# Optimization experiments

Hardware: AMD Instinct MI355X
Metric: run time of the kernel (lower is better)

## Reference

```python
import jax, jax.numpy as jnp
import numpy as np

N_NODES = 50000
N_EDGES = 800000
HEADS = 5
NFEAT = 5
C1 = 32  # hidden_layers


def setup_inputs() -> dict:
    key = jax.random.key(0)
    ks = jax.random.split(key, 20)
    s = 0.3  # glorot-ish scale
    d = {
        "x": jax.random.normal(ks[0], (N_NODES, NFEAT), jnp.float32),
        "edge_attr": jax.random.uniform(ks[1], (N_EDGES, 1), jnp.float32),
        "src": jax.random.randint(ks[2], (N_EDGES,), 0, N_NODES, jnp.int32),
        "dst": jax.random.randint(ks[3], (N_EDGES,), 0, N_NODES, jnp.int32),
        # conv1: in=5 -> heads=5, out=32, concat
        "W1": jax.random.normal(ks[4], (NFEAT, HEADS * C1), jnp.float32) * s,
        "a_src1": jax.random.normal(ks[5], (HEADS, C1), jnp.float32) * s,
        "a_dst1": jax.random.normal(ks[6], (HEADS, C1), jnp.float32) * s,
        "We1": jax.random.normal(ks[7], (1, HEADS * C1), jnp.float32) * s,
        "ae1": jax.random.normal(ks[8], (HEADS, C1), jnp.float32) * s,
        "b1": jnp.zeros((HEADS * C1,), jnp.float32),
        # conv2: in=160 -> heads=5, out=1, mean over heads
        "W2": jax.random.normal(ks[9], (HEADS * C1, HEADS * 1), jnp.float32) * 0.08,
        "a_src2": jax.random.normal(ks[10], (HEADS, 1), jnp.float32) * s,
        "a_dst2": jax.random.normal(ks[11], (HEADS, 1), jnp.float32) * s,
        "We2": jax.random.normal(ks[12], (1, HEADS * 1), jnp.float32) * s,
        "ae2": jax.random.normal(ks[13], (HEADS, 1), jnp.float32) * s,
        "b2": jnp.zeros((1,), jnp.float32),
        "Wlin": jax.random.normal(ks[14], (1, 1), jnp.float32),
    }
    return d


def gat_layer(x, src, dst, eattr, W, a_src, a_dst, We, a_e, bias, concat, n_nodes):
    """PyG GATConv with edge_dim, self-loops already added by caller."""
    H, C = a_src.shape
    h = (x @ W).reshape(-1, H, C)                      # [N,H,C]
    alpha_s = (h * a_src[None]).sum(-1)                # [N,H]
    alpha_d = (h * a_dst[None]).sum(-1)                # [N,H]
    ee = (eattr @ We).reshape(-1, H, C)                # [E,H,C]
    alpha_e = (ee * a_e[None]).sum(-1)                 # [E,H]
    logits = jax.nn.leaky_relu(alpha_s[src] + alpha_d[dst] + alpha_e, 0.2)
    # segment softmax over destination nodes
    m = jax.ops.segment_max(logits, dst, num_segments=n_nodes)
    m = jnp.where(jnp.isfinite(m), m, 0.0)
    ex = jnp.exp(logits - m[dst])
    denom = jax.ops.segment_sum(ex, dst, num_segments=n_nodes)
    alpha = ex / (denom[dst] + 1e-16)                  # [E,H]
    msg = (alpha[:, :, None] * h[src]).reshape(-1, H * C)
    agg = jax.ops.segment_sum(msg, dst, num_segments=n_nodes).reshape(n_nodes, H, C)
    if concat:
        return agg.reshape(n_nodes, H * C) + bias
    return agg.mean(axis=1) + bias


def reference(x, edge_attr, src, dst, W1, a_src1, a_dst1, We1, ae1, b1,
              W2, a_src2, a_dst2, We2, ae2, b2, Wlin):
    n = x.shape[0]
    loop = jnp.arange(n, dtype=src.dtype)
    s = jnp.concatenate([src, loop])
    t = jnp.concatenate([dst, loop])
    # self-loop edge_attr = mean of edge_attr (PyG fill_value='mean')
    ea_loop = jnp.broadcast_to(edge_attr.mean(axis=0, keepdims=True), (n, edge_attr.shape[1]))
    ea = jnp.concatenate([edge_attr, ea_loop], axis=0)

    x1 = gat_layer(x, s, t, ea, W1, a_src1, a_dst1, We1, ae1, b1, True, n)
    x2 = jax.nn.relu(x1)
    # dropout p=0.2 is identity in eval mode
    x4 = gat_layer(x2, s, t, ea, W2, a_src2, a_dst2, We2, ae2, b2, False, n)
    x5 = x4 @ Wlin                                     # Linear(1,1,bias=False)
    return jax.nn.sigmoid(x5)                          # [N,1]
```

## Files before the change

kernel.cpp:

```cpp
#include <hip/hip_runtime.h>
#include <hip/hip_fp16.h>
#include <math.h>

#define N_NODES 50000
#define N_EDGES 800000
#define E2 (N_EDGES + N_NODES)
#define HEADS 5
#define C1 32
#define F1 160

#define BSZ 64
#define NBK 782
#define NBL 128
#define CH  6641
#define MTOT (NBK*NBL)
#define MC  391
#define GRID_H1 (N_NODES/4)
#define CAP 1408

#define AGG1_NPB 32
#define AGG1_NB  1563

static constexpr size_t alignup(size_t x){ return (x + 255) & ~size_t(255); }
static constexpr size_t OFF_SCAL  = 0;
static constexpr size_t OFF_H     = alignup(OFF_SCAL + 64*4);
static constexpr size_t OFF_EAS   = alignup(OFF_H    + (size_t)MTOT*4);
static constexpr size_t OFF_PART  = alignup(OFF_EAS  + (size_t)NBL*4);
static constexpr size_t OFF_PPREF = alignup(OFF_PART + (size_t)MC*4);
static constexpr size_t OFF_BST   = alignup(OFF_PPREF+ (size_t)MC*4);
static constexpr size_t OFF_OFFS  = alignup(OFF_BST  + (size_t)(NBK+1)*4);
static constexpr size_t OFF_BPACK = alignup(OFF_OFFS + (size_t)(N_NODES+1)*4);
static constexpr size_t OFF_EDG   = alignup(OFF_BPACK+ (size_t)E2*8);
static constexpr size_t OFF_AS1P  = alignup(OFF_EDG  + (size_t)E2*4);
static constexpr size_t OFF_AD1P  = alignup(OFF_AS1P + (size_t)N_NODES*8*4);
static constexpr size_t OFF_G16   = alignup(OFF_AD1P + (size_t)N_NODES*8*4);
static constexpr size_t OFF_AD2P  = alignup(OFF_G16  + (size_t)N_NODES*16*2);
static constexpr size_t OFF_H1Q   = alignup(OFF_AD2P + (size_t)N_NODES*8*4);
static constexpr size_t OFF_X2H   = alignup(OFF_H1Q  + (size_t)N_NODES*F1);

typedef float vf2 __attribute__((ext_vector_type(2)));
__device__ __forceinline__ float4 fp8x4_to_f32(unsigned int r){
  vf2 lo = __builtin_amdgcn_cvt_pk_f32_fp8((int)r, false);
  vf2 hi = __builtin_amdgcn_cvt_pk_f32_fp8((int)r, true);
  return make_float4(lo.x, lo.y, hi.x, hi.y);
}

__global__ __launch_bounds__(320) void k_init(const float* __restrict__ x, const float* __restrict__ W1,
                       const float* __restrict__ as1w, const float* __restrict__ ad1w,
                       unsigned short* __restrict__ h1qh, float* __restrict__ as1ph, float* __restrict__ ad1ph,
                       const int* __restrict__ dst, const float* __restrict__ ea,
                       int* __restrict__ H, float* __restrict__ easum){
  __shared__ float sW[5*F1];
  int t = threadIdx.x;
  if (blockIdx.x < GRID_H1){
    for (int k = t; k < 5*F1; k += 320) sW[k] = W1[k];
    __syncthreads();
    int nl = t / 80;
    int c  = t - nl*80;
    int n  = blockIdx.x*4 + nl;
    int c0 = 2*c;
    float hv0 = 0.f, hv1 = 0.f;
    #pragma unroll
    for (int f = 0; f < 5; f++){
      float xv = x[n*5 + f];
      hv0 += xv * sW[f*F1 + c0];
      hv1 += xv * sW[f*F1 + c0 + 1];
    }
    int pk = __builtin_amdgcn_cvt_pk_fp8_f32(hv0, hv1, 0, false);
    int hh = c >> 4, pp = c & 15;
    h1qh[(size_t)hh*(N_NODES*16) + n*16 + pp] = (unsigned short)(pk & 0xFFFF);
    float vs = hv0*as1w[c0] + hv1*as1w[c0+1];
    float vd = hv0*ad1w[c0] + hv1*ad1w[c0+1];
    #pragma unroll
    for (int m = 8; m >= 1; m >>= 1){
      vs += __shfl_xor(vs, m, 64);
      vd += __shfl_xor(vd, m, 64);
    }
    if ((c & 15) == 0){
      int h = c >> 4;
      as1ph[h*N_NODES + n] = vs;
      ad1ph[h*N_NODES + n] = vd;
    }
  } else {
    int* hist = (int*)sW;
    float* wsum = (float*)&hist[NBK + 1];
    for (int k = t; k < NBK; k += 320) hist[k] = 0;
    __syncthreads();
    int b = blockIdx.x - GRID_H1;
    int e0 = b*CH, e1 = min(e0 + CH, E2);
    float s = 0.f;
    for (int e = e0 + t; e < e1; e += 320){
      int d;
      if (e < N_EDGES){ d = dst[e]; s += ea[e]; }
      else d = e - N_EDGES;
      atomicAdd(&hist[d >> 6], 1);
    }
    #pragma unroll
    for (int m = 1; m < 64; m <<= 1) s += __shfl_xor(s, m, 64);
    if ((t & 63) == 0) wsum[t >> 6] = s;
    __syncthreads();
    for (int k = t; k < NBK; k += 320) H[(size_t)k*NBL + b] = hist[k];
    if (t == 0) easum[b] = wsum[0] + wsum[1] + wsum[2] + wsum[3] + wsum[4];
  }
}

__global__ void k_s1(const int* __restrict__ H, int* __restrict__ partial){
  int i = blockIdx.x*256 + threadIdx.x;
  int v = (i < MTOT) ? H[i] : 0;
  #pragma unroll
  for (int m = 1; m < 64; m <<= 1) v += __shfl_xor(v, m, 64);
  __shared__ int sh[4];
  if ((threadIdx.x & 63) == 0) sh[threadIdx.x >> 6] = v;
  __syncthreads();
  if (threadIdx.x == 0) partial[blockIdx.x] = sh[0] + sh[1] + sh[2] + sh[3];
}

__global__ __launch_bounds__(512) void k_s2p(const int* __restrict__ partial, int* __restrict__ ppref,
                      int* __restrict__ offs, int* __restrict__ bstart,
                      const float* __restrict__ easum,
                      const float* __restrict__ We1, const float* __restrict__ ae1,
                      const float* __restrict__ We2, const float* __restrict__ ae2,
                      float* __restrict__ scal){
  __shared__ int sp[512];
  __shared__ float sh_ea[NBL];
  int t = threadIdx.x;
  if (t < NBL) sh_ea[t] = easum[t];
  if (t >= 448 && t < 448 + HEADS){
    int h = t - 448;
    float s = 0.f;
    for (int c = 0; c < C1; c++) s += We1[h*C1 + c] * ae1[h*C1 + c];
    scal[2 + h] = s;
    scal[7 + h] = We2[h] * ae2[h];
  }
  int v = (t < MC) ? partial[t] : 0;
  sp[t] = v;
  __syncthreads();
  if (t == 511){
    float es = 0.f;
    for (int i = 0; i < NBL; i++) es += sh_ea[i];
    scal[1] = es / (float)N_EDGES;
  }
  for (int off = 1; off < 512; off <<= 1){
    int u = (t >= off) ? sp[t - off] : 0;
    __syncthreads();
    sp[t] += u;
    __syncthreads();
  }
  if (t < MC) ppref[t] = sp[t] - v;
  if (t == 0){ offs[N_NODES] = E2; bstart[NBK] = E2; }
}

__global__ void k_s3(int* __restrict__ H, const int* __restrict__ ppref, int* __restrict__ bstart){
  __shared__ int sp[256];
  int b = blockIdx.x, t = threadIdx.x;
  int i = b*256 + t;
  int v = (i < MTOT) ? H[i] : 0;
  sp[t] = v;
  __syncthreads();
  for (int off = 1; off < 256; off <<= 1){
    int u = (t >= off) ? sp[t - off] : 0;
    __syncthreads();
    sp[t] += u;
    __syncthreads();
  }
  int P = ppref[b] + sp[t] - v;
  if (i < MTOT){
    H[i] = P;
    if (i % NBL == 0) bstart[i / NBL] = P;
  }
}

__global__ __launch_bounds__(256) void k_scat(const int* __restrict__ src, const int* __restrict__ dst,
                       const float* __restrict__ ea, const float* __restrict__ scal,
                       const int* __restrict__ H, int2* __restrict__ bpack){
  __shared__ int lofs[NBK];
  int b = blockIdx.x;
  for (int k = threadIdx.x; k < NBK; k += 256) lofs[k] = H[(size_t)k*NBL + b];
  __syncthreads();
  float mean = scal[1];
  int e0 = b*CH, e1 = min(e0 + CH, E2);
  for (int e = e0 + threadIdx.x; e < e1; e += 256){
    int d, s; float a;
    if (e < N_EDGES){ d = dst[e]; s = src[e]; a = ea[e]; }
    else { d = s = e - N_EDGES; a = mean; }
    int pos = atomicAdd(&lofs[d >> 6], 1);
    bpack[pos] = make_int2(s | ((d & 63) << 16), __float_as_int(a));
  }
}

__global__ __launch_bounds__(256) void k_final2(const int* __restrict__ bstart,
                        const int2* __restrict__ bpack,
                        int* __restrict__ offs, unsigned int* __restrict__ edge2){
  __shared__ int cnt[BSZ], cur[BSZ];
  __shared__ unsigned int s_edge[CAP];
  int k = blockIdx.x, t = threadIdx.x;
  int base = k*BSZ;
  if (t < BSZ) cnt[t] = 0;
  __syncthreads();
  int r0 = bstart[k], r1 = bstart[k + 1];
  int sz = r1 - r0;
  for (int j = r0 + t; j < r1; j += 256) atomicAdd(&cnt[(bpack[j].x >> 16) & 63], 1);
  __syncthreads();
  if (t == 0){
    int run = 0;
    for (int i = 0; i < BSZ; i++){ int c = cnt[i]; cnt[i] = run; cur[i] = run; run += c; }
  }
  __syncthreads();
  if (t < BSZ){
    int n = base + t;
    if (n < N_NODES) offs[n] = r0 + cnt[t];
  }
  if (sz <= CAP){
    for (int j = r0 + t; j < r1; j += 256){
      int2 v = bpack[j];
      int lp = atomicAdd(&cur[(v.x >> 16) & 63], 1);
      s_edge[lp] = (unsigned int)(v.x & 0xFFFF) |
                   ((unsigned int)__half_as_ushort(__float2half(__int_as_float(v.y))) << 16);
    }
    __syncthreads();
    for (int i = t; i < sz; i += 256) edge2[r0 + i] = s_edge[i];
  } else {
    for (int j = r0 + t; j < r1; j += 256){
      int2 v = bpack[j];
      int pos = r0 + atomicAdd(&cur[(v.x >> 16) & 63], 1);
      edge2[pos] = (unsigned int)(v.x & 0xFFFF) |
                   ((unsigned int)__half_as_ushort(__float2half(__int_as_float(v.y))) << 16);
    }
  }
}

__global__ __launch_bounds__(256) void k_agg1(const int* __restrict__ offs,
                      const unsigned int* __restrict__ edge2,
                      const float* __restrict__ as1ph, const float* __restrict__ ad1ph,
                      const float* __restrict__ scal,
                      const unsigned short* __restrict__ h1qh,
                      const float* __restrict__ b1, __half* __restrict__ x2h){
  int head = blockIdx.x / AGG1_NB;
  int nb   = blockIdx.x - head*AGG1_NB;
  int gl   = threadIdx.x >> 3;
  int q    = threadIdx.x & 7;
  int n    = nb*AGG1_NPB + gl;
  if (n >= N_NODES) return;
  float wd  = scal[2 + head];
  float adn = ad1ph[head*N_NODES + n];
  const float* asn = as1ph + head*N_NODES;
  const unsigned int* h1row = (const unsigned int*)h1qh + (size_t)head*(N_NODES*8) + q;
  int j0 = offs[n], j1 = offs[n + 1];
  float a0 = 0.f, a1 = 0.f, a2 = 0.f, a3 = 0.f, den = 0.f;
  int j = j0;
  for (; j + 7 < j1; j += 8){
    uint4 sa = *(const uint4*)(edge2 + j);
    uint4 sb = *(const uint4*)(edge2 + j + 4);
    unsigned int e0 = sa.x, e1 = sa.y, e2v = sa.z, e3 = sa.w;
    unsigned int e4 = sb.x, e5 = sb.y, e6 = sb.z, e7 = sb.w;
    int s0 = e0 & 0xFFFF, s1 = e1 & 0xFFFF, s2 = e2v & 0xFFFF, s3 = e3 & 0xFFFF;
    int s4 = e4 & 0xFFFF, s5 = e5 & 0xFFFF, s6 = e6 & 0xFFFF, s7 = e7 & 0xFFFF;
    unsigned int r0 = h1row[s0*8];
    unsigned int r1 = h1row[s1*8];
    unsigned int r2 = h1row[s2*8];
    unsigned int r3 = h1row[s3*8];
    unsigned int r4 = h1row[s4*8];
    unsigned int r5 = h1row[s5*8];
    unsigned int r6 = h1row[s6*8];
    unsigned int r7 = h1row[s7*8];
    float g0 = asn[s0], g1 = asn[s1];
    float g2 = asn[s2], g3 = asn[s3];
    float g4 = asn[s4], g5 = asn[s5];
    float g6 = asn[s6], g7 = asn[s7];
    float c0 = __half2float(__ushort_as_half((unsigned short)(e0 >> 16)));
    float c1 = __half2float(__ushort_as_half((unsigned short)(e1 >> 16)));
    float c2 = __half2float(__ushort_as_half((unsigned short)(e2v >> 16)));
    float c3 = __half2float(__ushort_as_half((unsigned short)(e3 >> 16)));
    float c4v = __half2float(__ushort_as_half((unsigned short)(e4 >> 16)));
    float c5v = __half2float(__ushort_as_half((unsigned short)(e5 >> 16)));
    float c6 = __half2float(__ushort_as_half((unsigned short)(e6 >> 16)));
    float c7 = __half2float(__ushort_as_half((unsigned short)(e7 >> 16)));
    float l0 = g0 + adn + c0*wd;  l0 = fminf(fmaxf(l0, 0.2f*l0), 10.f);
    float l1 = g1 + adn + c1*wd;  l1 = fminf(fmaxf(l1, 0.2f*l1), 10.f);
    float l2 = g2 + adn + c2*wd;  l2 = fminf(fmaxf(l2, 0.2f*l2), 10.f);
    float l3 = g3 + adn + c3*wd;  l3 = fminf(fmaxf(l3, 0.2f*l3), 10.f);
    float l4 = g4 + adn + c4v*wd; l4 = fminf(fmaxf(l4, 0.2f*l4), 10.f);
    float l5 = g5 + adn + c5v*wd; l5 = fminf(fmaxf(l5, 0.2f*l5), 10.f);
    float l6 = g6 + adn + c6*wd;  l6 = fminf(fmaxf(l6, 0.2f*l6), 10.f);
    float l7 = g7 + adn + c7*wd;  l7 = fminf(fmaxf(l7, 0.2f*l7), 10.f);
    float p0 = __expf(l0), p1 = __expf(l1), p2 = __expf(l2), p3 = __expf(l3);
    float p4 = __expf(l4), p5 = __expf(l5), p6 = __expf(l6), p7 = __expf(l7);
    den += p0 + p1 + p2 + p3 + p4 + p5 + p6 + p7;
    float4 f0 = fp8x4_to_f32(r0), f1 = fp8x4_to_f32(r1);
    float4 f2 = fp8x4_to_f32(r2), f3 = fp8x4_to_f32(r3);
    float4 f4 = fp8x4_to_f32(r4), f5 = fp8x4_to_f32(r5);
    float4 f6 = fp8x4_to_f32(r6), f7 = fp8x4_to_f32(r7);
    a0 += p0*f0.x; a1 += p0*f0.y; a2 += p0*f0.z; a3 += p0*f0.w;
    a0 += p1*f1.x; a1 += p1*f1.y; a2 += p1*f1.z; a3 += p1*f1.w;
    a0 += p2*f2.x; a1 += p2*f2.y; a2 += p2*f2.z; a3 += p2*f2.w;
    a0 += p3*f3.x; a1 += p3*f3.y; a2 += p3*f3.z; a3 += p3*f3.w;
    a0 += p4*f4.x; a1 += p4*f4.y; a2 += p4*f4.z; a3 += p4*f4.w;
    a0 += p5*f5.x; a1 += p5*f5.y; a2 += p5*f5.z; a3 += p5*f5.w;
    a0 += p6*f6.x; a1 += p6*f6.y; a2 += p6*f6.z; a3 += p6*f6.w;
    a0 += p7*f7.x; a1 += p7*f7.y; a2 += p7*f7.z; a3 += p7*f7.w;
  }
  for (; j < j1; ++j){
    unsigned int e = edge2[j];
    int s = e & 0xFFFF;
    float c = __half2float(__ushort_as_half((unsigned short)(e >> 16)));
    float g = asn[s];
    float lg = g + adn + c*wd;
    lg = fminf(fmaxf(lg, 0.2f*lg), 10.f);
    float p = __expf(lg);
    den += p;
    float4 f = fp8x4_to_f32(h1row[s*8]);
    a0 += p*f.x; a1 += p*f.y; a2 += p*f.z; a3 += p*f.w;
  }
  float inv = 1.f / (den + 1e-16f);
  float4 bb = *(const float4*)(b1 + head*C1 + 4*q);
  float v0 = fmaxf(a0*inv + bb.x, 0.f);
  float v1 = fmaxf(a1*inv + bb.y, 0.f);
  float v2 = fmaxf(a2*inv + bb.z, 0.f);
  float v3 = fmaxf(a3*inv + bb.w, 0.f);
  __half2 o0 = __floats2half2_rn(v0, v1);
  __half2 o1 = __floats2half2_rn(v2, v3);
  *(uint2*)(x2h + (size_t)n*F1 + head*C1 + 4*q) =
      make_uint2(*(unsigned int*)&o0, *(unsigned int*)&o1);
}

__global__ __launch_bounds__(256) void k_h2(const __half* __restrict__ x2h, const float* __restrict__ W2,
                    const float* __restrict__ asw2, const float* __restrict__ adw2,
                    __half* __restrict__ G16, float* __restrict__ ad2p){
  __shared__ float sW[F1*HEADS];
  for (int k = threadIdx.x; k < F1*HEADS; k += 256) sW[k] = W2[k];
  __syncthreads();
  int w = threadIdx.x >> 6, l = threadIdx.x & 63;
  int n = blockIdx.x*4 + w;
  const __half2* x22 = (const __half2*)x2h;
  float acc[HEADS] = {0.f, 0.f, 0.f, 0.f, 0.f};
  for (int k2 = l; k2 < 80; k2 += 64){
    float2 f = __half22float2(x22[(size_t)n*80 + k2]);
    #pragma unroll
    for (int h = 0; h < HEADS; h++)
      acc[h] += f.x * sW[(2*k2)*HEADS + h] + f.y * sW[(2*k2+1)*HEADS + h];
  }
  #pragma unroll
  for (int m = 1; m < 64; m <<= 1){
    #pragma unroll
    for (int h = 0; h < HEADS; h++) acc[h] += __shfl_xor(acc[h], m, 64);
  }
  if (l == 0){
    #pragma unroll
    for (int h = 0; h < HEADS; h++){
      G16[(size_t)n*16 + h]     = __float2half(acc[h]);
      G16[(size_t)n*16 + 5 + h] = __float2half(acc[h] * asw2[h]);
      ad2p[n*8 + h]             = acc[h] * adw2[h];
    }
    #pragma unroll
    for (int z = 10; z < 16; z++) G16[(size_t)n*16 + z] = __float2half(0.f);
  }
}

__global__ __launch_bounds__(256) void k_agg2(const int* __restrict__ offs,
                      const unsigned int* __restrict__ edge2,
                      const __half* __restrict__ G16, const float* __restrict__ ad2p,
                      const float* __restrict__ scal,
                      const float* __restrict__ b2, const float* __restrict__ Wlin,
                      float* __restrict__ out){
  int grp = threadIdx.x >> 4;
  int l16 = threadIdx.x & 15;
  int n = blockIdx.x*16 + grp;
  float adn[HEADS], wd[HEADS];
  #pragma unroll
  for (int h = 0; h < HEADS; h++){ adn[h] = ad2p[n*8 + h]; wd[h] = scal[7 + h]; }
  int j0 = offs[n], j1 = offs[n + 1];

  float den[HEADS] = {0,0,0,0,0};
  float ac[HEADS]  = {0,0,0,0,0};
  for (int j = j0 + l16; j < j1; j += 16){
    unsigned int e = edge2[j];
    int s = e & 0xFFFF;
    float c = __half2float(__ushort_as_half((unsigned short)(e >> 16)));
    const __half* gs = G16 + (size_t)s*16;
    union { uint4 u; __half2 h[4]; } U; U.u = *(const uint4*)gs;
    union { uint2 u; __half2 h[2]; } V; V.u = *(const uint2*)(gs + 8);
    float2 p01 = __half22float2(U.h[0]);
    float2 p23 = __half22float2(U.h[1]);
    float2 p45 = __half22float2(U.h[2]);
    float2 p67 = __half22float2(U.h[3]);
    float2 p89 = __half22float2(V.h[0]);
    float hv[HEADS] = {p01.x, p01.y, p23.x, p23.y, p45.x};
    float av[HEADS] = {p45.y, p67.x, p67.y, p89.x, p89.y};
    #pragma unroll
    for (int h = 0; h < HEADS; h++){
      float lg = av[h] + adn[h] + c*wd[h];
      lg = fmaxf(lg, 0.2f*lg);
      lg = fminf(lg, 50.f);
      float p = __expf(lg);
      den[h] += p;
      ac[h]  += p * hv[h];
    }
  }
  #pragma unroll
  for (int m = 1; m < 16; m <<= 1){
    #pragma unroll
    for (int h = 0; h < HEADS; h++){
      den[h] += __shfl_xor(den[h], m, 16);
      ac[h]  += __shfl_xor(ac[h], m, 16);
    }
  }
  if (l16 == 0){
    float v = 0.f;
    #pragma unroll
    for (int h = 0; h < HEADS; h++) v += ac[h] / (den[h] + 1e-16f);
    v = v * (1.f/HEADS) + b2[0];
    v *= Wlin[0];
    out[n] = 1.f / (1.f + __expf(-v));
  }
}

extern "C" void kernel_launch(void* const* d_in, const int* in_sizes, int n_in,
                              void* d_out, int out_size, void* d_ws, size_t ws_size,
                              hipStream_t stream) {
  const float* x    = (const float*)d_in[0];
  const float* ea   = (const float*)d_in[1];
  const int*   src  = (const int*)d_in[2];
  const int*   dst  = (const int*)d_in[3];
  const float* W1   = (const float*)d_in[4];
  const float* as1w = (const float*)d_in[5];
  const float* ad1w = (const float*)d_in[6];
  const float* We1  = (const float*)d_in[7];
  const float* ae1  = (const float*)d_in[8];
  const float* b1   = (const float*)d_in[9];
  const float* W2   = (const float*)d_in[10];
  const float* as2w = (const float*)d_in[11];
  const float* ad2w = (const float*)d_in[12];
  const float* We2  = (const float*)d_in[13];
  const float* ae2  = (const float*)d_in[14];
  const float* b2   = (const float*)d_in[15];
  const float* Wlin = (const float*)d_in[16];

  char* ws = (char*)d_ws;
  float* scal   = (float*)(ws + OFF_SCAL);
  int*   H      = (int*)  (ws + OFF_H);
  float* easum  = (float*)(ws + OFF_EAS);
  int*   part   = (int*)  (ws + OFF_PART);
  int*   ppref  = (int*)  (ws + OFF_PPREF);
  int*   bstart = (int*)  (ws + OFF_BST);
  int*   offs   = (int*)  (ws + OFF_OFFS);
  int2*  bpack  = (int2*) (ws + OFF_BPACK);
  unsigned int* edge2 = (unsigned int*)(ws + OFF_EDG);
  float* as1ph  = (float*)(ws + OFF_AS1P);
  float* ad1ph  = (float*)(ws + OFF_AD1P);
  __half* G16   = (__half*)(ws + OFF_G16);
  float* ad2p   = (float*)(ws + OFF_AD2P);
  unsigned short* h1qh = (unsigned short*)(ws + OFF_H1Q);
  __half* x2h   = (__half*)(ws + OFF_X2H);
  float* outp   = (float*)d_out;

  k_init   <<<GRID_H1 + NBL, 320, 0, stream>>>(x, W1, as1w, ad1w, h1qh, as1ph, ad1ph,
                                               dst, ea, H, easum);
  k_s1     <<<MC, 256, 0, stream>>>(H, part);
  k_s2p    <<<1, 512, 0, stream>>>(part, ppref, offs, bstart, easum, We1, ae1, We2, ae2, scal);
  k_s3     <<<MC, 256, 0, stream>>>(H, ppref, bstart);
  k_scat   <<<NBL, 256, 0, stream>>>(src, dst, ea, scal, H, bpack);
  k_final2 <<<NBK, 256, 0, stream>>>(bstart, bpack, offs, edge2);

  k_agg1   <<<HEADS*AGG1_NB, 256, 0, stream>>>(offs, edge2, as1ph, ad1ph, scal, h1qh, b1, x2h);
  k_h2     <<<N_NODES/4, 256, 0, stream>>>(x2h, W2, as2w, ad2w, G16, ad2p);
  k_agg2   <<<N_NODES/16, 256, 0, stream>>>(offs, edge2, G16, ad2p, scal, b2, Wlin, outp);
}
```

Baseline: 225.9 us.

## Precompute per-edge attention weights for all heads in a separate logit kernel

Adds a k_logit kernel that computes exp(leaky_relu logits) for all five heads once per edge. It stores them as fp16 packed with the source index in per-head edge arrays, reusing the bpack region and a new P2 buffer. k_agg1 then reads the precomputed weights instead of gathering alpha_src and recomputing exp per head. Per-node alpha values are stored as packed fp16 rows of 8, so one 16-byte load fetches all heads. The trade is an extra kernel launch, about 17MB of extra writes and reads, and fp16 rounding of the attention weights and alpha values.

```diff
diff --git a/kernel.cpp b/kernel.cpp
--- a/kernel.cpp
+++ b/kernel.cpp
@@ -31,12 +31,13 @@
 static constexpr size_t OFF_OFFS  = alignup(OFF_BST  + (size_t)(NBK+1)*4);
 static constexpr size_t OFF_BPACK = alignup(OFF_OFFS + (size_t)(N_NODES+1)*4);
 static constexpr size_t OFF_EDG   = alignup(OFF_BPACK+ (size_t)E2*8);
-static constexpr size_t OFF_AS1P  = alignup(OFF_EDG  + (size_t)E2*4);
-static constexpr size_t OFF_AD1P  = alignup(OFF_AS1P + (size_t)N_NODES*8*4);
-static constexpr size_t OFF_G16   = alignup(OFF_AD1P + (size_t)N_NODES*8*4);
+static constexpr size_t OFF_AS16  = alignup(OFF_EDG  + (size_t)E2*4);
+static constexpr size_t OFF_AD16  = alignup(OFF_AS16 + (size_t)N_NODES*8*2);
+static constexpr size_t OFF_G16   = alignup(OFF_AD16 + (size_t)N_NODES*8*2);
 static constexpr size_t OFF_AD2P  = alignup(OFF_G16  + (size_t)N_NODES*16*2);
 static constexpr size_t OFF_H1Q   = alignup(OFF_AD2P + (size_t)N_NODES*8*4);
 static constexpr size_t OFF_X2H   = alignup(OFF_H1Q  + (size_t)N_NODES*F1);
+static constexpr size_t OFF_P2    = alignup(OFF_X2H  + (size_t)N_NODES*F1*2);
 
 typedef float vf2 __attribute__((ext_vector_type(2)));
 __device__ __forceinline__ float4 fp8x4_to_f32(unsigned int r){
@@ -47,7 +48,7 @@
 
 __global__ __launch_bounds__(320) void k_init(const float* __restrict__ x, const float* __restrict__ W1,
                        const float* __restrict__ as1w, const float* __restrict__ ad1w,
-                       unsigned short* __restrict__ h1qh, float* __restrict__ as1ph, float* __restrict__ ad1ph,
+                       unsigned short* __restrict__ h1qh, __half* __restrict__ as16, __half* __restrict__ ad16,
                        const int* __restrict__ dst, const float* __restrict__ ea,
                        int* __restrict__ H, float* __restrict__ easum){
   __shared__ float sW[5*F1];
@@ -78,8 +79,8 @@
     }
     if ((c & 15) == 0){
       int h = c >> 4;
-      as1ph[h*N_NODES + n] = vs;
-      ad1ph[h*N_NODES + n] = vd;
+      as16[n*8 + h] = __float2half(vs);
+      ad16[n*8 + h] = __float2half(vd);
     }
   } else {
     int* hist = (int*)sW;
@@ -229,10 +230,47 @@
   }
 }
 
+__global__ __launch_bounds__(256) void k_logit(const int* __restrict__ offs,
+                      const unsigned int* __restrict__ edge2,
+                      const __half* __restrict__ as16, const __half* __restrict__ ad16,
+                      const float* __restrict__ scal,
+                      unsigned int* __restrict__ P01, unsigned int* __restrict__ P2){
+  int gl = threadIdx.x >> 3;
+  int q  = threadIdx.x & 7;
+  int n  = blockIdx.x*AGG1_NPB + gl;
+  if (n >= N_NODES) return;
+  union { uint4 u; __half2 h[4]; } AD; AD.u = *(const uint4*)(ad16 + (size_t)n*8);
+  float ad0 = __low2float(AD.h[0]), ad1 = __high2float(AD.h[0]);
+  float ad2 = __low2float(AD.h[1]), ad3 = __high2float(AD.h[1]);
+  float ad4 = __low2float(AD.h[2]);
+  float wd0 = scal[2], wd1 = scal[3], wd2 = scal[4], wd3 = scal[5], wd4 = scal[6];
+  int j0 = offs[n], j1 = offs[n + 1];
+  for (int j = j0 + q; j < j1; j += 8){
+    unsigned int e = edge2[j];
+    unsigned int lo = e & 0xFFFFu;
+    int s = (int)lo;
+    float c = __half2float(__ushort_as_half((unsigned short)(e >> 16)));
+    union { uint4 u; __half2 h[4]; } AS; AS.u = *(const uint4*)(as16 + (size_t)s*8);
+    float l0 = __low2float(AS.h[0])  + ad0 + c*wd0;  l0 = fminf(fmaxf(l0, 0.2f*l0), 10.f);
+    float l1 = __high2float(AS.h[0]) + ad1 + c*wd1;  l1 = fminf(fmaxf(l1, 0.2f*l1), 10.f);
+    float l2 = __low2float(AS.h[1])  + ad2 + c*wd2;  l2 = fminf(fmaxf(l2, 0.2f*l2), 10.f);
+    float l3 = __high2float(AS.h[1]) + ad3 + c*wd3;  l3 = fminf(fmaxf(l3, 0.2f*l3), 10.f);
+    float l4 = __low2float(AS.h[2])  + ad4 + c*wd4;  l4 = fminf(fmaxf(l4, 0.2f*l4), 10.f);
+    unsigned int p0 = (unsigned int)__half_as_ushort(__float2half(__expf(l0)));
+    unsigned int p1 = (unsigned int)__half_as_ushort(__float2half(__expf(l1)));
+    unsigned int p2 = (unsigned int)__half_as_ushort(__float2half(__expf(l2)));
+    unsigned int p3 = (unsigned int)__half_as_ushort(__float2half(__expf(l3)));
+    unsigned int p4 = (unsigned int)__half_as_ushort(__float2half(__expf(l4)));
+    P01[j]                  = lo | (p0 << 16);
+    P01[(size_t)E2 + j]     = lo | (p1 << 16);
+    P2[j]                   = lo | (p2 << 16);
+    P2[(size_t)E2 + j]      = lo | (p3 << 16);
+    P2[(size_t)2*E2 + j]    = lo | (p4 << 16);
+  }
+}
+
 __global__ __launch_bounds__(256) void k_agg1(const int* __restrict__ offs,
-                      const unsigned int* __restrict__ edge2,
-                      const float* __restrict__ as1ph, const float* __restrict__ ad1ph,
-                      const float* __restrict__ scal,
+                      const unsigned int* __restrict__ P01, const unsigned int* __restrict__ P2,
                       const unsigned short* __restrict__ h1qh,
                       const float* __restrict__ b1, __half* __restrict__ x2h){
   int head = blockIdx.x / AGG1_NB;
@@ -241,16 +279,15 @@
   int q    = threadIdx.x & 7;
   int n    = nb*AGG1_NPB + gl;
   if (n >= N_NODES) return;
-  float wd  = scal[2 + head];
-  float adn = ad1ph[head*N_NODES + n];
-  const float* asn = as1ph + head*N_NODES;
+  const unsigned int* EP = (head < 2) ? (P01 + (size_t)head*E2)
+                                      : (P2  + (size_t)(head-2)*E2);
   const unsigned int* h1row = (const unsigned int*)h1qh + (size_t)head*(N_NODES*8) + q;
   int j0 = offs[n], j1 = offs[n + 1];
   float a0 = 0.f, a1 = 0.f, a2 = 0.f, a3 = 0.f, den = 0.f;
   int j = j0;
   for (; j + 7 < j1; j += 8){
-    uint4 sa = *(const uint4*)(edge2 + j);
-    uint4 sb = *(const uint4*)(edge2 + j + 4);
+    uint4 sa = *(const uint4*)(EP + j);
+    uint4 sb = *(const uint4*)(EP + j + 4);
     unsigned int e0 = sa.x, e1 = sa.y, e2v = sa.z, e3 = sa.w;
     unsigned int e4 = sb.x, e5 = sb.y, e6 = sb.z, e7 = sb.w;
     int s0 = e0 & 0xFFFF, s1 = e1 & 0xFFFF, s2 = e2v & 0xFFFF, s3 = e3 & 0xFFFF;
@@ -263,29 +300,15 @@
     unsigned int r5 = h1row[s5*8];
     unsigned int r6 = h1row[s6*8];
     unsigned int r7 = h1row[s7*8];
-    float g0 = asn[s0], g1 = asn[s1];
-    float g2 = asn[s2], g3 = asn[s3];
-    float g4 = asn[s4], g5 = asn[s5];
-    float g6 = asn[s6], g7 = asn[s7];
-    float c0 = __half2float(__ushort_as_half((unsigned short)(e0 >> 16)));
-    float c1 = __half2float(__ushort_as_half((unsigned short)(e1 >> 16)));
-    float c2 = __half2float(__ushort_as_half((unsigned short)(e2v >> 16)));
-    float c3 = __half2float(__ushort_as_half((unsigned short)(e3 >> 16)));
-    float c4v = __half2float(__ushort_as_half((unsigned short)(e4 >> 16)));
-    float c5v = __half2float(__ushort_as_half((unsigned short)(e5 >> 16)));
-    float c6 = __half2float(__ushort_as_half((unsigned short)(e6 >> 16)));
-    float c7 = __half2float(__ushort_as_half((unsigned short)(e7 >> 16)));
-    float l0 = g0 + adn + c0*wd;  l0 = fminf(fmaxf(l0, 0.2f*l0), 10.f);
-    float l1 = g1 + adn + c1*wd;  l1 = fminf(fmaxf(l1, 0.2f*l1), 10.f);
-    float l2 = g2 + adn + c2*wd;  l2 = fminf(fmaxf(l2, 0.2f*l2), 10.f);
-    float l3 = g3 + adn + c3*wd;  l3 = fminf(fmaxf(l3, 0.2f*l3), 10.f);
-    float l4 = g4 + adn + c4v*wd; l4 = fminf(fmaxf(l4, 0.2f*l4), 10.f);
-    float l5 = g5 + adn + c5v*wd; l5 = fminf(fmaxf(l5, 0.2f*l5), 10.f);
-    float l6 = g6 + adn + c6*wd;  l6 = fminf(fmaxf(l6, 0.2f*l6), 10.f);
-    float l7 = g7 + adn + c7*wd;  l7 = fminf(fmaxf(l7, 0.2f*l7), 10.f);
-    float p0 = __expf(l0), p1 = __expf(l1), p2 = __expf(l2), p3 = __expf(l3);
-    float p4 = __expf(l4), p5 = __expf(l5), p6 = __expf(l6), p7 = __expf(l7);
-    den += p0 + p1 + p2 + p3 + p4 + p5 + p6 + p7;
+    float p0 = __half2float(__ushort_as_half((unsigned short)(e0 >> 16)));
+    float p1 = __half2float(__ushort_as_half((unsigned short)(e1 >> 16)));
+    float p2 = __half2float(__ushort_as_half((unsigned short)(e2v >> 16)));
+    float p3 = __half2float(__ushort_as_half((unsigned short)(e3 >> 16)));
+    float p4 = __half2float(__ushort_as_half((unsigned short)(e4 >> 16)));
+    float p5 = __half2float(__ushort_as_half((unsigned short)(e5 >> 16)));
+    float p6 = __half2float(__ushort_as_half((unsigned short)(e6 >> 16)));
+    float p7 = __half2float(__ushort_as_half((unsigned short)(e7 >> 16)));
+    den += ((p0 + p1) + (p2 + p3)) + ((p4 + p5) + (p6 + p7));
     float4 f0 = fp8x4_to_f32(r0), f1 = fp8x4_to_f32(r1);
     float4 f2 = fp8x4_to_f32(r2), f3 = fp8x4_to_f32(r3);
     float4 f4 = fp8x4_to_f32(r4), f5 = fp8x4_to_f32(r5);
@@ -300,13 +323,9 @@
     a0 += p7*f7.x; a1 += p7*f7.y; a2 += p7*f7.z; a3 += p7*f7.w;
   }
   for (; j < j1; ++j){
-    unsigned int e = edge2[j];
+    unsigned int e = EP[j];
     int s = e & 0xFFFF;
-    float c = __half2float(__ushort_as_half((unsigned short)(e >> 16)));
-    float g = asn[s];
-    float lg = g + adn + c*wd;
-    lg = fminf(fmaxf(lg, 0.2f*lg), 10.f);
-    float p = __expf(lg);
+    float p = __half2float(__ushort_as_half((unsigned short)(e >> 16)));
     den += p;
     float4 f = fp8x4_to_f32(h1row[s*8]);
     a0 += p*f.x; a1 += p*f.y; a2 += p*f.z; a3 += p*f.w;
@@ -444,16 +463,18 @@
   int*   bstart = (int*)  (ws + OFF_BST);
   int*   offs   = (int*)  (ws + OFF_OFFS);
   int2*  bpack  = (int2*) (ws + OFF_BPACK);
+  unsigned int* P01 = (unsigned int*)(ws + OFF_BPACK);
+  unsigned int* P2  = (unsigned int*)(ws + OFF_P2);
   unsigned int* edge2 = (unsigned int*)(ws + OFF_EDG);
-  float* as1ph  = (float*)(ws + OFF_AS1P);
-  float* ad1ph  = (float*)(ws + OFF_AD1P);
+  __half* as16  = (__half*)(ws + OFF_AS16);
+  __half* ad16  = (__half*)(ws + OFF_AD16);
   __half* G16   = (__half*)(ws + OFF_G16);
   float* ad2p   = (float*)(ws + OFF_AD2P);
   unsigned short* h1qh = (unsigned short*)(ws + OFF_H1Q);
   __half* x2h   = (__half*)(ws + OFF_X2H);
   float* outp   = (float*)d_out;
 
-  k_init   <<<GRID_H1 + NBL, 320, 0, stream>>>(x, W1, as1w, ad1w, h1qh, as1ph, ad1ph,
+  k_init   <<<GRID_H1 + NBL, 320, 0, stream>>>(x, W1, as1w, ad1w, h1qh, as16, ad16,
                                                dst, ea, H, easum);
   k_s1     <<<MC, 256, 0, stream>>>(H, part);
   k_s2p    <<<1, 512, 0, stream>>>(part, ppref, offs, bstart, easum, We1, ae1, We2, ae2, scal);
@@ -461,7 +482,8 @@
   k_scat   <<<NBL, 256, 0, stream>>>(src, dst, ea, scal, H, bpack);
   k_final2 <<<NBK, 256, 0, stream>>>(bstart, bpack, offs, edge2);
 
-  k_agg1   <<<HEADS*AGG1_NB, 256, 0, stream>>>(offs, edge2, as1ph, ad1ph, scal, h1qh, b1, x2h);
+  k_logit  <<<AGG1_NB, 256, 0, stream>>>(offs, edge2, as16, ad16, scal, P01, P2);
+  k_agg1   <<<HEADS*AGG1_NB, 256, 0, stream>>>(offs, P01, P2, h1qh, b1, x2h);
   k_h2     <<<N_NODES/4, 256, 0, stream>>>(x2h, W2, as2w, ad2w, G16, ad2p);
   k_agg2   <<<N_NODES/16, 256, 0, stream>>>(offs, edge2, G16, ad2p, scal, b2, Wlin, outp);
 }
```

Measured after the change: 224.1 us. About the same (-0.8%).
